# Optimization experiments

Hardware: AMD Instinct MI355X
Metric: run time of the kernel (lower is better)

The kernel has to match this reference:

```python
import jax, jax.numpy as jnp
import numpy as np
from jax import lax


def _make_grid():
    # Faithful replication of the torch buffer construction in __init__.
    r = np.arange(-128, 128) * np.pi / 256.0
    X, Y = np.meshgrid(r, r, indexing='ij')            # torch.meshgrid default 'ij'
    grid = np.tile(np.stack([X, Y], 0), (16, 1, 1))    # [32,256,256] channels x,y,x,y,...
    scales = 2.0 ** np.repeat(np.arange(16) / 2.0, 2)  # [32]: f0,f0,f1,f1,...
    grid = np.sin(grid * scales[:, None, None])
    return jnp.asarray(grid.reshape(32, 256 * 256).T, dtype=jnp.float32)  # [65536,32]

IMG_GRID = _make_grid()


def _conv_lrelu(x, w, b, padding, groups):
    y = lax.conv_general_dilated(x, w, (1, 1), padding,
                                 feature_group_count=groups,
                                 dimension_numbers=('NCHW', 'OIHW', 'NCHW'))
    return jax.nn.leaky_relu(y + b[None, :, None, None])


def _wn_linear(x, v, g, b):
    # nn.utils.weight_norm(Linear): w = g * v / ||v||  (norm over input dim, per output row)
    w = v * (g / jnp.linalg.norm(v, axis=1))[:, None]
    return x @ w.T + b


def _mem_stack(x, vf, gf, bf, vg, gg, bg):
    # memcnn AdditiveCoupling: x1,x2 = chunk(x,2); y1 = x1 + Fm(x2); y2 = x2 + Gm(y1)
    def step(h, p):
        pvf, pgf, pbf, pvg, pgg, pbg = p
        h1, h2 = jnp.split(h, 2, axis=-1)
        y1 = h1 + jax.nn.leaky_relu(_wn_linear(h2, pvf, pgf, pbf))
        y2 = h2 + jax.nn.leaky_relu(_wn_linear(y1, pvg, pgg, pbg))
        return jnp.concatenate([y1, y2], axis=-1), None
    h, _ = lax.scan(step, x, (vf, gf, bf, vg, gg, bg))
    return h


def _forward(feature, cw1, cb1, cw2, cb2, cw3, cb3, cw4, cb4, cw5, cb5,
             w1, b1, m1_vf, m1_gf, m1_bf, m1_vg, m1_gg, m1_bg,
             w2, b2, m2_vf, m2_gf, m2_bf, m2_vg, m2_gg, m2_bg, w3, b3):
    B = feature.shape[0]
    h = _conv_lrelu(feature, cw1, cb1, 'SAME', 4)
    h = _conv_lrelu(h, cw2, cb2, 'SAME', 3)
    h = _conv_lrelu(h, cw3, cb3, 'SAME', 2)
    h = _conv_lrelu(h, cw4, cb4, 'VALID', 3)
    h = _conv_lrelu(h, cw5, cb5, 'VALID', 1)   # [B,128,4,4]
    feat = h.reshape(B, -1)                    # [B,2048]
    N = IMG_GRID.shape[0]                      # 65536 coords, fully vectorized (no python chunk loop)
    grid_b = jnp.broadcast_to(IMG_GRID[None], (B, N, 32))
    x = jnp.concatenate([grid_b, jnp.broadcast_to(feat[:, None, :], (B, N, feat.shape[1]))], -1)
    mid = jax.nn.leaky_relu(x @ w1.T + b1)     # [B,N,1024]
    mid = _mem_stack(mid, m1_vf, m1_gf, m1_bf, m1_vg, m1_gg, m1_bg)
    h2 = jax.nn.leaky_relu(jnp.concatenate([grid_b, mid], -1) @ w2.T + b2)  # [B,N,512]
    h2 = _mem_stack(h2, m2_vf, m2_gf, m2_bf, m2_vg, m2_gg, m2_bg)
    rgb = jax.nn.sigmoid(h2 @ w3.T + b3)       # [B,N,3]
    img = rgb.transpose(0, 2, 1).reshape(B, 3, 256, 256)
    return img * 1.1 - 0.05


def setup_inputs() -> dict:
    key = jax.random.key(0)
    ks = iter(jax.random.split(key, 48))
    def nrm(shape, s=0.02):
        return jax.random.normal(next(ks), shape, jnp.float32) * s
    def gpar(shape):
        return jax.random.uniform(next(ks), shape, jnp.float32, 0.5, 1.0)
    inp = {}
    inp['feature'] = jax.random.normal(next(ks), (1, 1792, 8, 8), jnp.float32)
    inp['cw1'] = nrm((768, 448, 3, 3)); inp['cb1'] = nrm((768,), 0.01)   # groups=4: 1792/4=448
    inp['cw2'] = nrm((768, 256, 3, 3)); inp['cb2'] = nrm((768,), 0.01)   # groups=3
    inp['cw3'] = nrm((768, 384, 3, 3)); inp['cb3'] = nrm((768,), 0.01)   # groups=2
    inp['cw4'] = nrm((768, 256, 3, 3)); inp['cb4'] = nrm((768,), 0.01)   # groups=3, valid
    inp['cw5'] = nrm((128, 768, 3, 3)); inp['cb5'] = nrm((128,), 0.01)   # groups=1, valid
    inp['w1'] = nrm((1024, 2080)); inp['b1'] = nrm((1024,), 0.01)
    inp['m1_vf'] = nrm((8, 512, 512), 1.0); inp['m1_gf'] = gpar((8, 512)); inp['m1_bf'] = nrm((8, 512), 0.01)
    inp['m1_vg'] = nrm((8, 512, 512), 1.0); inp['m1_gg'] = gpar((8, 512)); inp['m1_bg'] = nrm((8, 512), 0.01)
    inp['w2'] = nrm((512, 1056)); inp['b2'] = nrm((512,), 0.01)
    inp['m2_vf'] = nrm((8, 256, 256), 1.0); inp['m2_gf'] = gpar((8, 256)); inp['m2_bf'] = nrm((8, 256), 0.01)
    inp['m2_vg'] = nrm((8, 256, 256), 1.0); inp['m2_gg'] = gpar((8, 256)); inp['m2_bg'] = nrm((8, 256), 0.01)
    inp['w3'] = nrm((3, 512)); inp['b3'] = nrm((3,), 0.01)
    return inp


def reference(feature, cw1, cb1, cw2, cb2, cw3, cb3, cw4, cb4, cw5, cb5,
              w1, b1, m1_vf, m1_gf, m1_bf, m1_vg, m1_gg, m1_bg,
              w2, b2, m2_vf, m2_gf, m2_bf, m2_vg, m2_gg, m2_bg, w3, b3):
    return _forward(feature, cw1, cb1, cw2, cb2, cw3, cb3, cw4, cb4, cw5, cb5,
                    w1, b1, m1_vf, m1_gf, m1_bf, m1_vg, m1_gg, m1_bg,
                    w2, b2, m2_vf, m2_gf, m2_bf, m2_vg, m2_gg, m2_bg, w3, b3)
```

## Files before the change

### kernel.cpp

```cpp
#include <hip/hip_runtime.h>
#include <cmath>

#define LRELU(x) fmaxf((x), 0.01f * (x))

typedef __attribute__((ext_vector_type(8))) short short8;
typedef __attribute__((ext_vector_type(4))) float f32x4;
typedef __attribute__((ext_vector_type(2))) unsigned uint2v;

constexpr int RS = 1032;

__device__ __forceinline__ unsigned short f2bf(float f) {
    return __builtin_bit_cast(unsigned short, (__bf16)f);
}
__device__ __forceinline__ float bf2f(unsigned short h) {
    return __uint_as_float((unsigned)h << 16);
}
__device__ __forceinline__ unsigned pk2(unsigned short a, unsigned short b) {
    return (unsigned)a | ((unsigned)b << 16);
}

__global__ void sgrid_kernel(float* __restrict__ sg) {
    int idx = blockIdx.x * blockDim.x + threadIdx.x;
    if (idx >= 256 * 32) return;
    int t = idx >> 5, c = idx & 31;
    double r = (double)(t - 128) * 3.14159265358979323846 / 256.0;
    double scale = exp2(0.5 * (double)(c >> 1));
    sg[idx] = (float)sin(r * scale);
}

__global__ __launch_bounds__(256) void conv_part(
    const float* __restrict__ x, const float* __restrict__ w,
    float* __restrict__ y, int Cin_g, int Cout_g, int Hin, int pad) {
    __shared__ float wsh[64 * 9];
    __shared__ float red[256];
    int oc = blockIdx.x, ch = blockIdx.y;
    int Hout = pad ? Hin : Hin - 2;
    int t = threadIdx.x;
    int ic0 = ch * 64;
    int nic = min(64, Cin_g - ic0);
    const float* wb = w + ((size_t)oc * Cin_g + ic0) * 9;
    for (int i = t; i < nic * 9; i += 256) wsh[i] = wb[i];
    __syncthreads();
    int p = t & 63, sub = t >> 6;
    int oy = p / Hout, ox = p % Hout;
    int g = oc / Cout_g;
    const float* xb = x + ((size_t)g * Cin_g + ic0) * Hin * Hin;
    bool valid = p < Hout * Hout;
    float acc = 0.f;
    if (valid) {
        for (int ic = sub; ic < nic; ic += 4) {
            const float* xc = xb + (size_t)ic * Hin * Hin;
            const float* wc = wsh + ic * 9;
            #pragma unroll
            for (int ky = 0; ky < 3; ++ky) {
                int iy = oy + ky - pad;
                if (iy < 0 || iy >= Hin) continue;
                #pragma unroll
                for (int kx = 0; kx < 3; ++kx) {
                    int ix = ox + kx - pad;
                    if (ix < 0 || ix >= Hin) continue;
                    acc = fmaf(xc[iy * Hin + ix], wc[ky * 3 + kx], acc);
                }
            }
        }
    }
    red[t] = acc;
    __syncthreads();
    if (t < 64 && valid)
        atomicAdd(&y[(size_t)oc * Hout * Hout + p],
                  red[t] + red[t + 64] + red[t + 128] + red[t + 192]);
}

__global__ void conv_finalize(float* __restrict__ y, const float* __restrict__ bias,
                              int HH, int n) {
    int i = blockIdx.x * 256 + threadIdx.x;
    if (i >= n) return;
    float v = y[i] + bias[i / HH];
    y[i] = LRELU(v);
}

__global__ void feat_c1_kernel(const float* __restrict__ feat, const float* __restrict__ w1,
                               const float* __restrict__ b1, float* __restrict__ c1) {
    int o = (blockIdx.x * blockDim.x + threadIdx.x) >> 6;
    int lane = threadIdx.x & 63;
    if (o >= 1024) return;
    const float* wr = w1 + (size_t)o * 2080 + 32;
    float sum = 0.f;
    for (int k = lane; k < 2048; k += 64) sum += feat[k] * wr[k];
    #pragma unroll
    for (int off = 32; off; off >>= 1) sum += __shfl_xor(sum, off);
    if (lane == 0) c1[o] = sum + b1[o];
}

__global__ __launch_bounds__(256) void wn_scale(const float* __restrict__ v, const float* __restrict__ g,
                                                float* __restrict__ s, int K) {
    __shared__ float red[256];
    int r = blockIdx.x, t = threadIdx.x;
    const float* vr = v + (size_t)r * K;
    float sum = 0.f;
    for (int k = t; k < K; k += 256) { float x = vr[k]; sum = fmaf(x, x, sum); }
    red[t] = sum;
    __syncthreads();
    for (int o = 128; o; o >>= 1) {
        if (t < o) red[t] += red[t + o];
        __syncthreads();
    }
    if (t == 0) s[r] = g[r] / sqrtf(red[0]);
}

__global__ void repack_kernel(const float* __restrict__ v, unsigned short* __restrict__ dst,
                              int T, int N, int K, int NT, int ldk, int koff) {
    int W = N / (NT * 16);
    int KC = K / 32;
    size_t total = (size_t)T * W * NT * KC * 64;
    size_t fi = (size_t)blockIdx.x * 256 + threadIdx.x;
    if (fi >= total) return;
    int l = fi & 63;
    size_t r = fi >> 6;
    int kc = r % KC; r /= KC;
    int nt = r % NT; r /= NT;
    int w  = r % W;  r /= W;
    int t  = (int)r;
    int n = w * NT * 16 + nt * 16 + (l & 15);
    int k = kc * 32 + (l >> 4) * 8;
    const float* src = v + ((size_t)t * N + n) * ldk + koff + k;
    unsigned short* d = dst + fi * 8;
    #pragma unroll
    for (int e = 0; e < 8; ++e) d[e] = f2bf(src[e]);
}

__global__ void repack_w2k(const float* __restrict__ w2, unsigned short* __restrict__ dst) {
    int fi = blockIdx.x * 256 + threadIdx.x;
    if (fi >= 65536) return;
    int l = fi & 63;
    int r = fi >> 6;
    int kc = r & 31; r >>= 5;
    int nt = r & 3;  r >>= 2;
    int w = r;
    int l15 = l & 15;
    int col = (nt < 2) ? (w * 32 + nt * 16 + l15) : (256 + w * 32 + (nt - 2) * 16 + l15);
    int k = kc * 32 + (l >> 4) * 8;
    const float* src = w2 + (size_t)col * 1056 + 32 + k;
    unsigned short* d = dst + (size_t)fi * 8;
    #pragma unroll
    for (int e = 0; e < 8; ++e) d[e] = f2bf(src[e]);
}

__global__ void pxy_kernel(const float* __restrict__ sg, const float* __restrict__ w1,
                           const float* __restrict__ c1, float* __restrict__ Px,
                           float* __restrict__ Py) {
    int idx = blockIdx.x * 256 + threadIdx.x;
    int t = idx >> 10, o = idx & 1023;
    const float* wr = w1 + (size_t)o * 2080;
    const float* sr = sg + t * 32;
    float px = 0.f, py = 0.f;
    #pragma unroll
    for (int k = 0; k < 16; ++k) {
        px = fmaf(sr[2 * k], wr[2 * k], px);
        py = fmaf(sr[2 * k + 1], wr[2 * k + 1], py);
    }
    Px[idx] = px + c1[o];
    Py[idx] = py;
}

__global__ void qxy_kernel(const float* __restrict__ sg, const float* __restrict__ w2,
                           float* __restrict__ Qx, float* __restrict__ Qy) {
    int idx = blockIdx.x * 256 + threadIdx.x;
    int t = idx >> 9, o = idx & 511;
    const float* wr = w2 + (size_t)o * 1056;
    const float* sr = sg + t * 32;
    float qx = 0.f, qy = 0.f;
    #pragma unroll
    for (int k = 0; k < 16; ++k) {
        qx = fmaf(sr[2 * k], wr[2 * k], qx);
        qy = fmaf(sr[2 * k + 1], wr[2 * k + 1], qy);
    }
    Qx[idx] = qx;
    Qy[idx] = qy;
}

__device__ __forceinline__ void step1(unsigned short* sm, int w, int l, int l15, int lq,
                                      int srcb, int dstb,
                                      const unsigned short* __restrict__ Bp,
                                      const float* __restrict__ sc,
                                      const float* __restrict__ bi,
                                      f32x4* master) {
    f32x4 acc[4][4] = {};
    const unsigned short* wb = Bp + (size_t)w * (4 * 16 * 512) + (size_t)l * 8;
    const unsigned short* abase = sm + (size_t)l15 * RS + srcb + lq * 8;
    short8 b0[4], b1[4];
    #pragma unroll
    for (int nt = 0; nt < 4; ++nt) b0[nt] = *(const short8*)(wb + (size_t)(nt * 16 + 0) * 512);
    #pragma unroll
    for (int nt = 0; nt < 4; ++nt) b1[nt] = *(const short8*)(wb + (size_t)(nt * 16 + 1) * 512);
    #pragma unroll
    for (int kc = 0; kc < 16; ++kc) {
        short8 bn[4];
        if (kc < 14) {
            #pragma unroll
            for (int nt = 0; nt < 4; ++nt)
                bn[nt] = *(const short8*)(wb + (size_t)(nt * 16 + kc + 2) * 512);
        }
        short8 af[4];
        #pragma unroll
        for (int mt = 0; mt < 4; ++mt)
            af[mt] = *(const short8*)(abase + (size_t)(mt * 16) * RS + kc * 32);
        #pragma unroll
        for (int mt = 0; mt < 4; ++mt)
            #pragma unroll
            for (int nt = 0; nt < 4; ++nt)
                acc[mt][nt] = __builtin_amdgcn_mfma_f32_16x16x32_bf16(b0[nt], af[mt], acc[mt][nt], 0, 0, 0);
        #pragma unroll
        for (int nt = 0; nt < 4; ++nt) { b0[nt] = b1[nt]; b1[nt] = bn[nt]; }
    }
    #pragma unroll
    for (int nt = 0; nt < 4; ++nt) {
        int nb = w * 64 + nt * 16 + lq * 4;
        float4 s4 = *(const float4*)(sc + nb);
        float4 bb = *(const float4*)(bi + nb);
        #pragma unroll
        for (int mt = 0; mt < 4; ++mt) {
            int row = mt * 16 + l15;
            f32x4 m = master[mt * 4 + nt];
            float v0 = LRELU(acc[mt][nt][0] * s4.x + bb.x) + m[0];
            float v1 = LRELU(acc[mt][nt][1] * s4.y + bb.y) + m[1];
            float v2 = LRELU(acc[mt][nt][2] * s4.z + bb.z) + m[2];
            float v3 = LRELU(acc[mt][nt][3] * s4.w + bb.w) + m[3];
            m[0] = v0; m[1] = v1; m[2] = v2; m[3] = v3;
            master[mt * 4 + nt] = m;
            uint2v hv; hv[0] = pk2(f2bf(v0), f2bf(v1)); hv[1] = pk2(f2bf(v2), f2bf(v3));
            *(uint2v*)(sm + (size_t)row * RS + dstb + nb) = hv;
        }
    }
}

__device__ __forceinline__ void step2(unsigned short* sm, int w, int l, int l15, int lq,
                                      int srcb, int dstb,
                                      const unsigned short* __restrict__ Bp,
                                      const float* __restrict__ sc,
                                      const float* __restrict__ bi,
                                      f32x4* master) {
    f32x4 acc[4][2] = {};
    const unsigned short* wb = Bp + (size_t)w * (2 * 8 * 512) + (size_t)l * 8;
    const unsigned short* abase = sm + (size_t)l15 * RS + srcb + lq * 8;
    short8 b0[2], b1[2];
    #pragma unroll
    for (int nt = 0; nt < 2; ++nt) b0[nt] = *(const short8*)(wb + (size_t)(nt * 8 + 0) * 512);
    #pragma unroll
    for (int nt = 0; nt < 2; ++nt) b1[nt] = *(const short8*)(wb + (size_t)(nt * 8 + 1) * 512);
    #pragma unroll
    for (int kc = 0; kc < 8; ++kc) {
        short8 bn[2];
        if (kc < 6) {
            #pragma unroll
            for (int nt = 0; nt < 2; ++nt)
                bn[nt] = *(const short8*)(wb + (size_t)(nt * 8 + kc + 2) * 512);
        }
        short8 af[4];
        #pragma unroll
        for (int mt = 0; mt < 4; ++mt)
            af[mt] = *(const short8*)(abase + (size_t)(mt * 16) * RS + kc * 32);
        #pragma unroll
        for (int mt = 0; mt < 4; ++mt)
            #pragma unroll
            for (int nt = 0; nt < 2; ++nt)
                acc[mt][nt] = __builtin_amdgcn_mfma_f32_16x16x32_bf16(b0[nt], af[mt], acc[mt][nt], 0, 0, 0);
        #pragma unroll
        for (int nt = 0; nt < 2; ++nt) { b0[nt] = b1[nt]; b1[nt] = bn[nt]; }
    }
    #pragma unroll
    for (int nt = 0; nt < 2; ++nt) {
        int nb = w * 32 + nt * 16 + lq * 4;
        float4 s4 = *(const float4*)(sc + nb);
        float4 bb = *(const float4*)(bi + nb);
        #pragma unroll
        for (int mt = 0; mt < 4; ++mt) {
            int row = mt * 16 + l15;
            f32x4 m = master[mt * 2 + nt];
            float v0 = LRELU(acc[mt][nt][0] * s4.x + bb.x) + m[0];
            float v1 = LRELU(acc[mt][nt][1] * s4.y + bb.y) + m[1];
            float v2 = LRELU(acc[mt][nt][2] * s4.z + bb.z) + m[2];
            float v3 = LRELU(acc[mt][nt][3] * s4.w + bb.w) + m[3];
            m[0] = v0; m[1] = v1; m[2] = v2; m[3] = v3;
            master[mt * 2 + nt] = m;
            uint2v hv; hv[0] = pk2(f2bf(v0), f2bf(v1)); hv[1] = pk2(f2bf(v2), f2bf(v3));
            *(uint2v*)(sm + (size_t)row * RS + dstb + nb) = hv;
        }
    }
}

__global__ __launch_bounds__(512, 2) void fused_mlp(
    const float* __restrict__ Px, const float* __restrict__ Py,
    const float* __restrict__ Qx, const float* __restrict__ Qy,
    const unsigned short* __restrict__ m1f, const float* __restrict__ s1f, const float* __restrict__ bf1,
    const unsigned short* __restrict__ m1g, const float* __restrict__ s1g, const float* __restrict__ bg1,
    const unsigned short* __restrict__ w2m, const float* __restrict__ b2,
    const unsigned short* __restrict__ m2f, const float* __restrict__ s2f, const float* __restrict__ bf2_,
    const unsigned short* __restrict__ m2g, const float* __restrict__ s2g, const float* __restrict__ bg2_,
    const float* __restrict__ w3, const float* __restrict__ b3,
    float* __restrict__ out) {
    extern __shared__ unsigned short sm[];
    int tid = threadIdx.x;
    int w = tid >> 6, l = tid & 63;
    int l15 = l & 15, lq = l >> 4;
    int n0 = blockIdx.x * 64;
    int i = n0 >> 8, jb = n0 & 255;

    f32x4 mh[32];

    #pragma unroll
    for (int h = 0; h < 2; ++h) {
        #pragma unroll
        for (int nt = 0; nt < 4; ++nt) {
            int nb = h * 512 + w * 64 + nt * 16 + lq * 4;
            float4 px4 = *(const float4*)(Px + (size_t)i * 1024 + nb);
            #pragma unroll
            for (int mt = 0; mt < 4; ++mt) {
                int row = mt * 16 + l15;
                float4 py4 = *(const float4*)(Py + (size_t)(jb + row) * 1024 + nb);
                f32x4 m;
                m[0] = LRELU(px4.x + py4.x);
                m[1] = LRELU(px4.y + py4.y);
                m[2] = LRELU(px4.z + py4.z);
                m[3] = LRELU(px4.w + py4.w);
                mh[h * 16 + mt * 4 + nt] = m;
                uint2v hv; hv[0] = pk2(f2bf(m[0]), f2bf(m[1])); hv[1] = pk2(f2bf(m[2]), f2bf(m[3]));
                *(uint2v*)(sm + (size_t)row * RS + nb) = hv;
            }
        }
    }
    __syncthreads();

    for (int t = 0; t < 8; ++t) {
        step1(sm, w, l, l15, lq, 512, 0, m1f + (size_t)t * 512 * 512, s1f + t * 512, bf1 + t * 512, mh);
        __syncthreads();
        step1(sm, w, l, l15, lq, 0, 512, m1g + (size_t)t * 512 * 512, s1g + t * 512, bg1 + t * 512, mh + 16);
        __syncthreads();
    }

    {
        f32x4 acc[4][4] = {};
        const unsigned short* wb = w2m + (size_t)w * (4 * 32 * 512) + (size_t)l * 8;
        const unsigned short* abase = sm + (size_t)l15 * RS + lq * 8;
        short8 b0[4], b1[4];
        #pragma unroll
        for (int nt = 0; nt < 4; ++nt) b0[nt] = *(const short8*)(wb + (size_t)(nt * 32 + 0) * 512);
        #pragma unroll
        for (int nt = 0; nt < 4; ++nt) b1[nt] = *(const short8*)(wb + (size_t)(nt * 32 + 1) * 512);
        #pragma unroll
        for (int kc = 0; kc < 32; ++kc) {
            short8 bn[4];
            if (kc < 30) {
                #pragma unroll
                for (int nt = 0; nt < 4; ++nt)
                    bn[nt] = *(const short8*)(wb + (size_t)(nt * 32 + kc + 2) * 512);
            }
            short8 af[4];
            #pragma unroll
            for (int mt = 0; mt < 4; ++mt)
                af[mt] = *(const short8*)(abase + (size_t)(mt * 16) * RS + kc * 32);
            #pragma unroll
            for (int mt = 0; mt < 4; ++mt)
                #pragma unroll
                for (int nt = 0; nt < 4; ++nt)
                    acc[mt][nt] = __builtin_amdgcn_mfma_f32_16x16x32_bf16(b0[nt], af[mt], acc[mt][nt], 0, 0, 0);
            #pragma unroll
            for (int nt = 0; nt < 4; ++nt) { b0[nt] = b1[nt]; b1[nt] = bn[nt]; }
        }
        __syncthreads();
        #pragma unroll
        for (int nt = 0; nt < 4; ++nt) {
            int colb = ((nt < 2) ? (w * 32 + nt * 16) : (256 + w * 32 + (nt - 2) * 16)) + lq * 4;
            float4 qx4 = *(const float4*)(Qx + (size_t)i * 512 + colb);
            float4 b24 = *(const float4*)(b2 + colb);
            #pragma unroll
            for (int mt = 0; mt < 4; ++mt) {
                int row = mt * 16 + l15;
                float4 qy4 = *(const float4*)(Qy + (size_t)(jb + row) * 512 + colb);
                f32x4 m;
                m[0] = LRELU(acc[mt][nt][0] + qx4.x + qy4.x + b24.x);
                m[1] = LRELU(acc[mt][nt][1] + qx4.y + qy4.y + b24.y);
                m[2] = LRELU(acc[mt][nt][2] + qx4.z + qy4.z + b24.z);
                m[3] = LRELU(acc[mt][nt][3] + qx4.w + qy4.w + b24.w);
                mh[(nt >> 1) * 16 + mt * 2 + (nt & 1)] = m;
                uint2v hv; hv[0] = pk2(f2bf(m[0]), f2bf(m[1])); hv[1] = pk2(f2bf(m[2]), f2bf(m[3]));
                *(uint2v*)(sm + (size_t)row * RS + colb) = hv;
            }
        }
    }
    __syncthreads();

    for (int t = 0; t < 8; ++t) {
        step2(sm, w, l, l15, lq, 256, 0, m2f + (size_t)t * 256 * 256, s2f + t * 256, bf2_ + t * 256, mh);
        __syncthreads();
        step2(sm, w, l, l15, lq, 0, 256, m2g + (size_t)t * 256 * 256, s2g + t * 256, bg2_ + t * 256, mh + 16);
        __syncthreads();
    }

    __syncthreads();
    {
        float* smf = (float*)sm;
        #pragma unroll
        for (int hh = 0; hh < 2; ++hh)
            #pragma unroll
            for (int nt = 0; nt < 2; ++nt) {
                int colb = hh * 256 + w * 32 + nt * 16 + lq * 4;
                #pragma unroll
                for (int mt = 0; mt < 4; ++mt) {
                    int row = mt * 16 + l15;
                    f32x4 m = mh[hh * 16 + mt * 2 + nt];
                    *(f32x4*)(smf + (size_t)row * (RS / 2) + colb) = m;
                }
            }
    }
    __syncthreads();
    {
        const float* smf = (const float*)sm;
        #pragma unroll
        for (int rr = 0; rr < 8; ++rr) {
            int row = w * 8 + rr;
            float s0 = 0.f, s1 = 0.f, s2 = 0.f;
            #pragma unroll
            for (int it = 0; it < 8; ++it) {
                int k = it * 64 + l;
                float hv = smf[(size_t)row * (RS / 2) + k];
                s0 = fmaf(hv, w3[k], s0);
                s1 = fmaf(hv, w3[512 + k], s1);
                s2 = fmaf(hv, w3[1024 + k], s2);
            }
            #pragma unroll
            for (int off = 32; off; off >>= 1) {
                s0 += __shfl_xor(s0, off);
                s1 += __shfl_xor(s1, off);
                s2 += __shfl_xor(s2, off);
            }
            if (l == 0) {
                float v[3] = {s0 + b3[0], s1 + b3[1], s2 + b3[2]};
                #pragma unroll
                for (int c = 0; c < 3; ++c) {
                    float sg = 1.0f / (1.0f + expf(-v[c]));
                    out[(size_t)c * 65536 + n0 + row] = 1.1f * sg - 0.05f;
                }
            }
        }
    }
}

extern "C" void kernel_launch(void* const* d_in, const int* in_sizes, int n_in,
                              void* d_out, int out_size, void* d_ws, size_t ws_size,
                              hipStream_t stream) {
    const float* feature = (const float*)d_in[0];
    const float* cw1 = (const float*)d_in[1];  const float* cb1 = (const float*)d_in[2];
    const float* cw2 = (const float*)d_in[3];  const float* cb2 = (const float*)d_in[4];
    const float* cw3 = (const float*)d_in[5];  const float* cb3 = (const float*)d_in[6];
    const float* cw4 = (const float*)d_in[7];  const float* cb4 = (const float*)d_in[8];
    const float* cw5 = (const float*)d_in[9];  const float* cb5 = (const float*)d_in[10];
    const float* w1  = (const float*)d_in[11]; const float* b1  = (const float*)d_in[12];
    const float* m1_vf = (const float*)d_in[13]; const float* m1_gf = (const float*)d_in[14];
    const float* m1_bf = (const float*)d_in[15];
    const float* m1_vg = (const float*)d_in[16]; const float* m1_gg = (const float*)d_in[17];
    const float* m1_bg = (const float*)d_in[18];
    const float* w2  = (const float*)d_in[19]; const float* b2  = (const float*)d_in[20];
    const float* m2_vf = (const float*)d_in[21]; const float* m2_gf = (const float*)d_in[22];
    const float* m2_bf = (const float*)d_in[23];
    const float* m2_vg = (const float*)d_in[24]; const float* m2_gg = (const float*)d_in[25];
    const float* m2_bg = (const float*)d_in[26];
    const float* w3  = (const float*)d_in[27]; const float* b3  = (const float*)d_in[28];
    float* out = (float*)d_out;

    float* ws = (float*)d_ws;
    size_t off = 0;
    float* sgrid   = ws + off; off += 256 * 32;
    float* cbA     = ws + off; off += 768 * 64;
    float* cbB     = ws + off; off += 768 * 64;
    float* featbuf = ws + off; off += 2048;
    float* c1      = ws + off; off += 1024;
    float* s1f     = ws + off; off += 8 * 512;
    float* s1g     = ws + off; off += 8 * 512;
    float* s2f     = ws + off; off += 8 * 256;
    float* s2g     = ws + off; off += 8 * 256;
    float* Px      = ws + off; off += 256 * 1024;
    float* Py      = ws + off; off += 256 * 1024;
    float* Qx      = ws + off; off += 256 * 512;
    float* Qy      = ws + off; off += 256 * 512;
    unsigned short* m1f_p = (unsigned short*)(ws + off); off += (size_t)8 * 512 * 512 / 2;
    unsigned short* m1g_p = (unsigned short*)(ws + off); off += (size_t)8 * 512 * 512 / 2;
    unsigned short* m2f_p = (unsigned short*)(ws + off); off += (size_t)8 * 256 * 256 / 2;
    unsigned short* m2g_p = (unsigned short*)(ws + off); off += (size_t)8 * 256 * 256 / 2;
    unsigned short* w2m_p = (unsigned short*)(ws + off); off += (size_t)512 * 1024 / 2;

    sgrid_kernel<<<32, 256, 0, stream>>>(sgrid);
    wn_scale<<<8 * 512, 256, 0, stream>>>(m1_vf, m1_gf, s1f, 512);
    wn_scale<<<8 * 512, 256, 0, stream>>>(m1_vg, m1_gg, s1g, 512);
    wn_scale<<<8 * 256, 256, 0, stream>>>(m2_vf, m2_gf, s2f, 256);
    wn_scale<<<8 * 256, 256, 0, stream>>>(m2_vg, m2_gg, s2g, 256);
    repack_kernel<<<1024, 256, 0, stream>>>(m1_vf, m1f_p, 8, 512, 512, 4, 512, 0);
    repack_kernel<<<1024, 256, 0, stream>>>(m1_vg, m1g_p, 8, 512, 512, 4, 512, 0);
    repack_kernel<<<256, 256, 0, stream>>>(m2_vf, m2f_p, 8, 256, 256, 2, 256, 0);
    repack_kernel<<<256, 256, 0, stream>>>(m2_vg, m2g_p, 8, 256, 256, 2, 256, 0);
    repack_w2k<<<256, 256, 0, stream>>>(w2, w2m_p);

    hipMemsetAsync(cbA, 0, 768 * 64 * sizeof(float), stream);
    conv_part<<<dim3(768, 7), 256, 0, stream>>>(feature, cw1, cbA, 448, 192, 8, 1);
    conv_finalize<<<(768 * 64) / 256, 256, 0, stream>>>(cbA, cb1, 64, 768 * 64);
    hipMemsetAsync(cbB, 0, 768 * 64 * sizeof(float), stream);
    conv_part<<<dim3(768, 4), 256, 0, stream>>>(cbA, cw2, cbB, 256, 256, 8, 1);
    conv_finalize<<<(768 * 64) / 256, 256, 0, stream>>>(cbB, cb2, 64, 768 * 64);
    hipMemsetAsync(cbA, 0, 768 * 64 * sizeof(float), stream);
    conv_part<<<dim3(768, 6), 256, 0, stream>>>(cbB, cw3, cbA, 384, 384, 8, 1);
    conv_finalize<<<(768 * 64) / 256, 256, 0, stream>>>(cbA, cb3, 64, 768 * 64);
    hipMemsetAsync(cbB, 0, 768 * 36 * sizeof(float), stream);
    conv_part<<<dim3(768, 4), 256, 0, stream>>>(cbA, cw4, cbB, 256, 256, 8, 0);
    conv_finalize<<<(768 * 36 + 255) / 256, 256, 0, stream>>>(cbB, cb4, 36, 768 * 36);
    hipMemsetAsync(featbuf, 0, 2048 * sizeof(float), stream);
    conv_part<<<dim3(128, 12), 256, 0, stream>>>(cbB, cw5, featbuf, 768, 128, 6, 0);
    conv_finalize<<<(2048 + 255) / 256, 256, 0, stream>>>(featbuf, cb5, 16, 2048);

    feat_c1_kernel<<<1024 / 4, 256, 0, stream>>>(featbuf, w1, b1, c1);
    pxy_kernel<<<(256 * 1024) / 256, 256, 0, stream>>>(sgrid, w1, c1, Px, Py);
    qxy_kernel<<<(256 * 512) / 256, 256, 0, stream>>>(sgrid, w2, Qx, Qy);

    size_t lds_bytes = (size_t)64 * RS * sizeof(unsigned short);
    hipFuncSetAttribute(reinterpret_cast<const void*>(fused_mlp),
                        hipFuncAttributeMaxDynamicSharedMemorySize, (int)lds_bytes);
    fused_mlp<<<1024, 512, lds_bytes, stream>>>(
        Px, Py, Qx, Qy,
        m1f_p, s1f, m1_bf, m1g_p, s1g, m1_bg,
        w2m_p, b2,
        m2f_p, s2f, m2_bf, m2g_p, s2g, m2_bg,
        w3, b3, out);
}
```

Measured before the change: 1.428 ms.

## Store fp32 residual stream as bf16 hi/lo pairs; merge setup kernels and memsets

The residual master copy of the coupling-block state in the fused MLP kernel changes from fp32 registers (32 f32x4) to a split bf16 hi+lo representation. For the first stack, the hi half sits in LDS and the lo half in packed registers. For the second stack, both halves sit in LDS, so the final projection reads them straight from shared memory with no fp32 staging pass. Setup kernels (weight-norm scales, repacks, P/Q precompute) are merged into single launches and the conv memsets collapse into one, cutting launch count. The aim is lower register pressure and fewer launches, at the cost of extra LDS traffic and pack/unpack ALU work per step, plus a small precision change from the two-bf16 approximation of fp32.

```diff
diff --git a/kernel.cpp b/kernel.cpp
--- a/kernel.cpp
+++ b/kernel.cpp
@@ -12,11 +12,25 @@
 __device__ __forceinline__ unsigned short f2bf(float f) {
     return __builtin_bit_cast(unsigned short, (__bf16)f);
 }
-__device__ __forceinline__ float bf2f(unsigned short h) {
-    return __uint_as_float((unsigned)h << 16);
-}
 __device__ __forceinline__ unsigned pk2(unsigned short a, unsigned short b) {
     return (unsigned)a | ((unsigned)b << 16);
+}
+__device__ __forceinline__ uint2v cvt4(f32x4 v) {
+    uint2v r;
+    r[0] = pk2(f2bf(v[0]), f2bf(v[1]));
+    r[1] = pk2(f2bf(v[2]), f2bf(v[3]));
+    return r;
+}
+__device__ __forceinline__ f32x4 unpk4(uint2v p) {
+    f32x4 r;
+    r[0] = __uint_as_float(p[0] << 16);
+    r[1] = __uint_as_float(p[0] & 0xffff0000u);
+    r[2] = __uint_as_float(p[1] << 16);
+    r[3] = __uint_as_float(p[1] & 0xffff0000u);
+    return r;
+}
+__device__ __forceinline__ f32x4 lrelu4(f32x4 v) {
+    return __builtin_elementwise_max(v, 0.01f * v);
 }
 
 __global__ void sgrid_kernel(float* __restrict__ sg) {
@@ -92,10 +106,18 @@
     if (lane == 0) c1[o] = sum + b1[o];
 }
 
-__global__ __launch_bounds__(256) void wn_scale(const float* __restrict__ v, const float* __restrict__ g,
-                                                float* __restrict__ s, int K) {
+__global__ __launch_bounds__(256) void wn_all(
+    const float* __restrict__ v1f, const float* __restrict__ g1f, float* __restrict__ s1f,
+    const float* __restrict__ v1g, const float* __restrict__ g1g, float* __restrict__ s1g,
+    const float* __restrict__ v2f, const float* __restrict__ g2f, float* __restrict__ s2f,
+    const float* __restrict__ v2g, const float* __restrict__ g2g, float* __restrict__ s2g) {
     __shared__ float red[256];
-    int r = blockIdx.x, t = threadIdx.x;
+    int b = blockIdx.x, t = threadIdx.x;
+    const float* v; const float* g; float* s; int K, r;
+    if (b < 4096)       { v = v1f; g = g1f; s = s1f; K = 512; r = b; }
+    else if (b < 8192)  { v = v1g; g = g1g; s = s1g; K = 512; r = b - 4096; }
+    else if (b < 10240) { v = v2f; g = g2f; s = s2f; K = 256; r = b - 8192; }
+    else                { v = v2g; g = g2g; s = s2g; K = 256; r = b - 10240; }
     const float* vr = v + (size_t)r * K;
     float sum = 0.f;
     for (int k = t; k < K; k += 256) { float x = vr[k]; sum = fmaf(x, x, sum); }
@@ -108,14 +130,10 @@
     if (t == 0) s[r] = g[r] / sqrtf(red[0]);
 }
 
-__global__ void repack_kernel(const float* __restrict__ v, unsigned short* __restrict__ dst,
-                              int T, int N, int K, int NT, int ldk, int koff) {
+__device__ __forceinline__ void repack_one(const float* __restrict__ v, unsigned short* __restrict__ dst,
+                                           int N, int NT, int KC, int ldk, int koff, size_t fi) {
     int W = N / (NT * 16);
-    int KC = K / 32;
-    size_t total = (size_t)T * W * NT * KC * 64;
-    size_t fi = (size_t)blockIdx.x * 256 + threadIdx.x;
-    if (fi >= total) return;
-    int l = fi & 63;
+    int l = (int)(fi & 63);
     size_t r = fi >> 6;
     int kc = r % KC; r /= KC;
     int nt = r % NT; r /= NT;
@@ -129,54 +147,52 @@
     for (int e = 0; e < 8; ++e) d[e] = f2bf(src[e]);
 }
 
-__global__ void repack_w2k(const float* __restrict__ w2, unsigned short* __restrict__ dst) {
-    int fi = blockIdx.x * 256 + threadIdx.x;
-    if (fi >= 65536) return;
-    int l = fi & 63;
-    int r = fi >> 6;
-    int kc = r & 31; r >>= 5;
-    int nt = r & 3;  r >>= 2;
-    int w = r;
-    int l15 = l & 15;
-    int col = (nt < 2) ? (w * 32 + nt * 16 + l15) : (256 + w * 32 + (nt - 2) * 16 + l15);
-    int k = kc * 32 + (l >> 4) * 8;
-    const float* src = w2 + (size_t)col * 1056 + 32 + k;
-    unsigned short* d = dst + (size_t)fi * 8;
-    #pragma unroll
-    for (int e = 0; e < 8; ++e) d[e] = f2bf(src[e]);
-}
-
-__global__ void pxy_kernel(const float* __restrict__ sg, const float* __restrict__ w1,
-                           const float* __restrict__ c1, float* __restrict__ Px,
-                           float* __restrict__ Py) {
+__global__ void repack_all(const float* __restrict__ m1vf, const float* __restrict__ m1vg,
+                           const float* __restrict__ m2vf, const float* __restrict__ m2vg,
+                           const float* __restrict__ w2,
+                           unsigned short* __restrict__ p1f, unsigned short* __restrict__ p1g,
+                           unsigned short* __restrict__ p2f, unsigned short* __restrict__ p2g,
+                           unsigned short* __restrict__ pw2) {
+    size_t fi = (size_t)blockIdx.x * 256 + threadIdx.x;
+    const size_t n1 = 262144, n2 = 65536;
+    if (fi < n1)                repack_one(m1vf, p1f, 512, 4, 16, 512, 0, fi);
+    else if (fi < 2 * n1)       repack_one(m1vg, p1g, 512, 4, 16, 512, 0, fi - n1);
+    else if (fi < 2 * n1 + n2)  repack_one(m2vf, p2f, 256, 2, 8, 256, 0, fi - 2 * n1);
+    else if (fi < 2 * n1 + 2 * n2) repack_one(m2vg, p2g, 256, 2, 8, 256, 0, fi - 2 * n1 - n2);
+    else                        repack_one(w2, pw2, 512, 4, 32, 1056, 32, fi - 2 * n1 - 2 * n2);
+}
+
+__global__ void pq_kernel(const float* __restrict__ sg, const float* __restrict__ w1,
+                          const float* __restrict__ c1, const float* __restrict__ w2,
+                          float* __restrict__ Px, float* __restrict__ Py,
+                          float* __restrict__ Qx, float* __restrict__ Qy) {
     int idx = blockIdx.x * 256 + threadIdx.x;
-    int t = idx >> 10, o = idx & 1023;
-    const float* wr = w1 + (size_t)o * 2080;
-    const float* sr = sg + t * 32;
-    float px = 0.f, py = 0.f;
-    #pragma unroll
-    for (int k = 0; k < 16; ++k) {
-        px = fmaf(sr[2 * k], wr[2 * k], px);
-        py = fmaf(sr[2 * k + 1], wr[2 * k + 1], py);
-    }
-    Px[idx] = px + c1[o];
-    Py[idx] = py;
-}
-
-__global__ void qxy_kernel(const float* __restrict__ sg, const float* __restrict__ w2,
-                           float* __restrict__ Qx, float* __restrict__ Qy) {
-    int idx = blockIdx.x * 256 + threadIdx.x;
-    int t = idx >> 9, o = idx & 511;
-    const float* wr = w2 + (size_t)o * 1056;
-    const float* sr = sg + t * 32;
-    float qx = 0.f, qy = 0.f;
-    #pragma unroll
-    for (int k = 0; k < 16; ++k) {
-        qx = fmaf(sr[2 * k], wr[2 * k], qx);
-        qy = fmaf(sr[2 * k + 1], wr[2 * k + 1], qy);
-    }
-    Qx[idx] = qx;
-    Qy[idx] = qy;
+    if (idx < 256 * 1024) {
+        int t = idx >> 10, o = idx & 1023;
+        const float* wr = w1 + (size_t)o * 2080;
+        const float* sr = sg + t * 32;
+        float px = 0.f, py = 0.f;
+        #pragma unroll
+        for (int k = 0; k < 16; ++k) {
+            px = fmaf(sr[2 * k], wr[2 * k], px);
+            py = fmaf(sr[2 * k + 1], wr[2 * k + 1], py);
+        }
+        Px[idx] = px + c1[o];
+        Py[idx] = py;
+    } else {
+        int j = idx - 256 * 1024;
+        int t = j >> 9, o = j & 511;
+        const float* wr = w2 + (size_t)o * 1056;
+        const float* sr = sg + t * 32;
+        float qx = 0.f, qy = 0.f;
+        #pragma unroll
+        for (int k = 0; k < 16; ++k) {
+            qx = fmaf(sr[2 * k], wr[2 * k], qx);
+            qy = fmaf(sr[2 * k + 1], wr[2 * k + 1], qy);
+        }
+        Qx[j] = qx;
+        Qy[j] = qy;
+    }
 }
 
 __device__ __forceinline__ void step1(unsigned short* sm, int w, int l, int l15, int lq,
@@ -184,7 +200,7 @@
                                       const unsigned short* __restrict__ Bp,
                                       const float* __restrict__ sc,
                                       const float* __restrict__ bi,
-                                      f32x4* master) {
+                                      uint2v* lo_half) {
     f32x4 acc[4][4] = {};
     const unsigned short* wb = Bp + (size_t)w * (4 * 16 * 512) + (size_t)l * 8;
     const unsigned short* abase = sm + (size_t)l15 * RS + srcb + lq * 8;
@@ -216,20 +232,18 @@
     #pragma unroll
     for (int nt = 0; nt < 4; ++nt) {
         int nb = w * 64 + nt * 16 + lq * 4;
-        float4 s4 = *(const float4*)(sc + nb);
-        float4 bb = *(const float4*)(bi + nb);
+        f32x4 s4 = *(const f32x4*)(sc + nb);
+        f32x4 bb = *(const f32x4*)(bi + nb);
         #pragma unroll
         for (int mt = 0; mt < 4; ++mt) {
             int row = mt * 16 + l15;
-            f32x4 m = master[mt * 4 + nt];
-            float v0 = LRELU(acc[mt][nt][0] * s4.x + bb.x) + m[0];
-            float v1 = LRELU(acc[mt][nt][1] * s4.y + bb.y) + m[1];
-            float v2 = LRELU(acc[mt][nt][2] * s4.z + bb.z) + m[2];
-            float v3 = LRELU(acc[mt][nt][3] * s4.w + bb.w) + m[3];
-            m[0] = v0; m[1] = v1; m[2] = v2; m[3] = v3;
-            master[mt * 4 + nt] = m;
-            uint2v hv; hv[0] = pk2(f2bf(v0), f2bf(v1)); hv[1] = pk2(f2bf(v2), f2bf(v3));
-            *(uint2v*)(sm + (size_t)row * RS + dstb + nb) = hv;
+            size_t hidx = (size_t)row * RS + dstb + nb;
+            uint2v hold = *(uint2v*)(sm + hidx);
+            f32x4 v = lrelu4(acc[mt][nt] * s4 + bb);
+            v += unpk4(hold) + unpk4(lo_half[mt * 4 + nt]);
+            uint2v hnew = cvt4(v);
+            *(uint2v*)(sm + hidx) = hnew;
+            lo_half[mt * 4 + nt] = cvt4(v - unpk4(hnew));
         }
     }
 }
@@ -238,8 +252,7 @@
                                       int srcb, int dstb,
                                       const unsigned short* __restrict__ Bp,
                                       const float* __restrict__ sc,
-                                      const float* __restrict__ bi,
-                                      f32x4* master) {
+                                      const float* __restrict__ bi) {
     f32x4 acc[4][2] = {};
     const unsigned short* wb = Bp + (size_t)w * (2 * 8 * 512) + (size_t)l * 8;
     const unsigned short* abase = sm + (size_t)l15 * RS + srcb + lq * 8;
@@ -271,20 +284,19 @@
     #pragma unroll
     for (int nt = 0; nt < 2; ++nt) {
         int nb = w * 32 + nt * 16 + lq * 4;
-        float4 s4 = *(const float4*)(sc + nb);
-        float4 bb = *(const float4*)(bi + nb);
+        f32x4 s4 = *(const f32x4*)(sc + nb);
+        f32x4 bb = *(const f32x4*)(bi + nb);
         #pragma unroll
         for (int mt = 0; mt < 4; ++mt) {
             int row = mt * 16 + l15;
-            f32x4 m = master[mt * 2 + nt];
-            float v0 = LRELU(acc[mt][nt][0] * s4.x + bb.x) + m[0];
-            float v1 = LRELU(acc[mt][nt][1] * s4.y + bb.y) + m[1];
-            float v2 = LRELU(acc[mt][nt][2] * s4.z + bb.z) + m[2];
-            float v3 = LRELU(acc[mt][nt][3] * s4.w + bb.w) + m[3];
-            m[0] = v0; m[1] = v1; m[2] = v2; m[3] = v3;
-            master[mt * 2 + nt] = m;
-            uint2v hv; hv[0] = pk2(f2bf(v0), f2bf(v1)); hv[1] = pk2(f2bf(v2), f2bf(v3));
-            *(uint2v*)(sm + (size_t)row * RS + dstb + nb) = hv;
+            size_t hidx = (size_t)row * RS + dstb + nb;
+            uint2v hold = *(uint2v*)(sm + hidx);
+            uint2v lold = *(uint2v*)(sm + hidx + 512);
+            f32x4 v = lrelu4(acc[mt][nt] * s4 + bb);
+            v += unpk4(hold) + unpk4(lold);
+            uint2v hnew = cvt4(v);
+            *(uint2v*)(sm + hidx) = hnew;
+            *(uint2v*)(sm + hidx + 512) = cvt4(v - unpk4(hnew));
         }
     }
 }
@@ -306,35 +318,31 @@
     int n0 = blockIdx.x * 64;
     int i = n0 >> 8, jb = n0 & 255;
 
-    f32x4 mh[32];
+    uint2v lo_pk[32];
 
     #pragma unroll
     for (int h = 0; h < 2; ++h) {
         #pragma unroll
         for (int nt = 0; nt < 4; ++nt) {
             int nb = h * 512 + w * 64 + nt * 16 + lq * 4;
-            float4 px4 = *(const float4*)(Px + (size_t)i * 1024 + nb);
+            f32x4 px4 = *(const f32x4*)(Px + (size_t)i * 1024 + nb);
             #pragma unroll
             for (int mt = 0; mt < 4; ++mt) {
                 int row = mt * 16 + l15;
-                float4 py4 = *(const float4*)(Py + (size_t)(jb + row) * 1024 + nb);
-                f32x4 m;
-                m[0] = LRELU(px4.x + py4.x);
-                m[1] = LRELU(px4.y + py4.y);
-                m[2] = LRELU(px4.z + py4.z);
-                m[3] = LRELU(px4.w + py4.w);
-                mh[h * 16 + mt * 4 + nt] = m;
-                uint2v hv; hv[0] = pk2(f2bf(m[0]), f2bf(m[1])); hv[1] = pk2(f2bf(m[2]), f2bf(m[3]));
+                f32x4 py4 = *(const f32x4*)(Py + (size_t)(jb + row) * 1024 + nb);
+                f32x4 v = lrelu4(px4 + py4);
+                uint2v hv = cvt4(v);
                 *(uint2v*)(sm + (size_t)row * RS + nb) = hv;
+                lo_pk[h * 16 + mt * 4 + nt] = cvt4(v - unpk4(hv));
             }
         }
     }
     __syncthreads();
 
     for (int t = 0; t < 8; ++t) {
-        step1(sm, w, l, l15, lq, 512, 0, m1f + (size_t)t * 512 * 512, s1f + t * 512, bf1 + t * 512, mh);
+        step1(sm, w, l, l15, lq, 512, 0, m1f + (size_t)t * 512 * 512, s1f + t * 512, bf1 + t * 512, lo_pk);
         __syncthreads();
-        step1(sm, w, l, l15, lq, 0, 512, m1g + (size_t)t * 512 * 512, s1g + t * 512, bg1 + t * 512, mh + 16);
+        step1(sm, w, l, l15, lq, 0, 512, m1g + (size_t)t * 512 * 512, s1g + t * 512, bg1 + t * 512, lo_pk + 16);
         __syncthreads();
     }
 
@@ -370,77 +378,56 @@
         __syncthreads();
         #pragma unroll
         for (int nt = 0; nt < 4; ++nt) {
-            int colb = ((nt < 2) ? (w * 32 + nt * 16) : (256 + w * 32 + (nt - 2) * 16)) + lq * 4;
-            float4 qx4 = *(const float4*)(Qx + (size_t)i * 512 + colb);
-            float4 b24 = *(const float4*)(b2 + colb);
+            int nb = w * 64 + nt * 16 + lq * 4;
+            f32x4 qx4 = *(const f32x4*)(Qx + (size_t)i * 512 + nb);
+            f32x4 b24 = *(const f32x4*)(b2 + nb);
             #pragma unroll
             for (int mt = 0; mt < 4; ++mt) {
                 int row = mt * 16 + l15;
-                float4 qy4 = *(const float4*)(Qy + (size_t)(jb + row) * 512 + colb);
-                f32x4 m;
-                m[0] = LRELU(acc[mt][nt][0] + qx4.x + qy4.x + b24.x);
-                m[1] = LRELU(acc[mt][nt][1] + qx4.y + qy4.y + b24.y);
-                m[2] = LRELU(acc[mt][nt][2] + qx4.z + qy4.z + b24.z);
-                m[3] = LRELU(acc[mt][nt][3] + qx4.w + qy4.w + b24.w);
-                mh[(nt >> 1) * 16 + mt * 2 + (nt & 1)] = m;
-                uint2v hv; hv[0] = pk2(f2bf(m[0]), f2bf(m[1])); hv[1] = pk2(f2bf(m[2]), f2bf(m[3]));
-                *(uint2v*)(sm + (size_t)row * RS + colb) = hv;
+                f32x4 qy4 = *(const f32x4*)(Qy + (size_t)(jb + row) * 512 + nb);
+                f32x4 v = lrelu4(acc[mt][nt] + qx4 + qy4 + b24);
+                uint2v hv = cvt4(v);
+                size_t hidx = (size_t)row * RS + nb;
+                *(uint2v*)(sm + hidx) = hv;
+                *(uint2v*)(sm + hidx + 512) = cvt4(v - unpk4(hv));
             }
         }
     }
     __syncthreads();
 
     for (int t = 0; t < 8; ++t) {
-        step2(sm, w, l, l15, lq, 256, 0, m2f + (size_t)t * 256 * 256, s2f + t * 256, bf2_ + t * 256, mh);
+        step2(sm, w, l, l15, lq, 256, 0, m2f + (size_t)t * 256 * 256, s2f + t * 256, bf2_ + t * 256);
         __syncthreads();
-        step2(sm, w, l, l15, lq, 0, 256, m2g + (size_t)t * 256 * 256, s2g + t * 256, bg2_ + t * 256, mh + 16);
+        step2(sm, w, l, l15, lq, 0, 256, m2g + (size_t)t * 256 * 256, s2g + t * 256, bg2_ + t * 256);
         __syncthreads();
     }
 
-    __syncthreads();
-    {
-        float* smf = (float*)sm;
-        #pragma unroll
-        for (int hh = 0; hh < 2; ++hh)
-            #pragma unroll
-            for (int nt = 0; nt < 2; ++nt) {
-                int colb = hh * 256 + w * 32 + nt * 16 + lq * 4;
-                #pragma unroll
-                for (int mt = 0; mt < 4; ++mt) {
-                    int row = mt * 16 + l15;
-                    f32x4 m = mh[hh * 16 + mt * 2 + nt];
-                    *(f32x4*)(smf + (size_t)row * (RS / 2) + colb) = m;
-                }
-            }
-    }
-    __syncthreads();
-    {
-        const float* smf = (const float*)sm;
-        #pragma unroll
-        for (int rr = 0; rr < 8; ++rr) {
-            int row = w * 8 + rr;
-            float s0 = 0.f, s1 = 0.f, s2 = 0.f;
-            #pragma unroll
-            for (int it = 0; it < 8; ++it) {
-                int k = it * 64 + l;
-                float hv = smf[(size_t)row * (RS / 2) + k];
-                s0 = fmaf(hv, w3[k], s0);
-                s1 = fmaf(hv, w3[512 + k], s1);
-                s2 = fmaf(hv, w3[1024 + k], s2);
-            }
-            #pragma unroll
-            for (int off = 32; off; off >>= 1) {
-                s0 += __shfl_xor(s0, off);
-                s1 += __shfl_xor(s1, off);
-                s2 += __shfl_xor(s2, off);
-            }
-            if (l == 0) {
-                float v[3] = {s0 + b3[0], s1 + b3[1], s2 + b3[2]};
-                #pragma unroll
-                for (int c = 0; c < 3; ++c) {
-                    float sg = 1.0f / (1.0f + expf(-v[c]));
-                    out[(size_t)c * 65536 + n0 + row] = 1.1f * sg - 0.05f;
-                }
+    #pragma unroll
+    for (int rr = 0; rr < 8; ++rr) {
+        int row = w * 8 + rr;
+        float s0 = 0.f, s1 = 0.f, s2 = 0.f;
+        #pragma unroll
+        for (int it = 0; it < 8; ++it) {
+            int k = it * 64 + l;
+            size_t hidx = (size_t)row * RS + k;
+            float hv = __uint_as_float((unsigned)sm[hidx] << 16) +
+                       __uint_as_float((unsigned)sm[hidx + 512] << 16);
+            s0 = fmaf(hv, w3[k], s0);
+            s1 = fmaf(hv, w3[512 + k], s1);
+            s2 = fmaf(hv, w3[1024 + k], s2);
+        }
+        #pragma unroll
+        for (int off = 32; off; off >>= 1) {
+            s0 += __shfl_xor(s0, off);
+            s1 += __shfl_xor(s1, off);
+            s2 += __shfl_xor(s2, off);
+        }
+        if (l == 0) {
+            float v[3] = {s0 + b3[0], s1 + b3[1], s2 + b3[2]};
+            #pragma unroll
+            for (int c = 0; c < 3; ++c) {
+                float sg = 1.0f / (1.0f + expf(-v[c]));
+                out[(size_t)c * 65536 + n0 + row] = 1.1f * sg - 0.05f;
             }
         }
     }
@@ -473,7 +460,10 @@
     float* sgrid   = ws + off; off += 256 * 32;
     float* cbA     = ws + off; off += 768 * 64;
     float* cbB     = ws + off; off += 768 * 64;
+    float* cbC     = ws + off; off += 768 * 64;
+    float* cbD     = ws + off; off += 768 * 36;
     float* featbuf = ws + off; off += 2048;
+    size_t convN   = 768 * 64 * 3 + 768 * 36 + 2048;
     float* c1      = ws + off; off += 1024;
     float* s1f     = ws + off; off += 8 * 512;
     float* s1g     = ws + off; off += 8 * 512;
@@ -490,35 +480,25 @@
     unsigned short* w2m_p = (unsigned short*)(ws + off); off += (size_t)512 * 1024 / 2;
 
     sgrid_kernel<<<32, 256, 0, stream>>>(sgrid);
-    wn_scale<<<8 * 512, 256, 0, stream>>>(m1_vf, m1_gf, s1f, 512);
-    wn_scale<<<8 * 512, 256, 0, stream>>>(m1_vg, m1_gg, s1g, 512);
-    wn_scale<<<8 * 256, 256, 0, stream>>>(m2_vf, m2_gf, s2f, 256);
-    wn_scale<<<8 * 256, 256, 0, stream>>>(m2_vg, m2_gg, s2g, 256);
-    repack_kernel<<<1024, 256, 0, stream>>>(m1_vf, m1f_p, 8, 512, 512, 4, 512, 0);
-    repack_kernel<<<1024, 256, 0, stream>>>(m1_vg, m1g_p, 8, 512, 512, 4, 512, 0);
-    repack_kernel<<<256, 256, 0, stream>>>(m2_vf, m2f_p, 8, 256, 256, 2, 256, 0);
-    repack_kernel<<<256, 256, 0, stream>>>(m2_vg, m2g_p, 8, 256, 256, 2, 256, 0);
-    repack_w2k<<<256, 256, 0, stream>>>(w2, w2m_p);
-
-    hipMemsetAsync(cbA, 0, 768 * 64 * sizeof(float), stream);
+    wn_all<<<12288, 256, 0, stream>>>(m1_vf, m1_gf, s1f, m1_vg, m1_gg, s1g,
+                                      m2_vf, m2_gf, s2f, m2_vg, m2_gg, s2g);
+    repack_all<<<2816, 256, 0, stream>>>(m1_vf, m1_vg, m2_vf, m2_vg, w2,
+                                         m1f_p, m1g_p, m2f_p, m2g_p, w2m_p);
+
+    hipMemsetAsync(cbA, 0, convN * sizeof(float), stream);
     conv_part<<<dim3(768, 7), 256, 0, stream>>>(feature, cw1, cbA, 448, 192, 8, 1);
     conv_finalize<<<(768 * 64) / 256, 256, 0, stream>>>(cbA, cb1, 64, 768 * 64);
-    hipMemsetAsync(cbB, 0, 768 * 64 * sizeof(float), stream);
     conv_part<<<dim3(768, 4), 256, 0, stream>>>(cbA, cw2, cbB, 256, 256, 8, 1);
     conv_finalize<<<(768 * 64) / 256, 256, 0, stream>>>(cbB, cb2, 64, 768 * 64);
-    hipMemsetAsync(cbA, 0, 768 * 64 * sizeof(float), stream);
-    conv_part<<<dim3(768, 6), 256, 0, stream>>>(cbB, cw3, cbA, 384, 384, 8, 1);
-    conv_finalize<<<(768 * 64) / 256, 256, 0, stream>>>(cbA, cb3, 64, 768 * 64);
-    hipMemsetAsync(cbB, 0, 768 * 36 * sizeof(float), stream);
-    conv_part<<<dim3(768, 4), 256, 0, stream>>>(cbA, cw4, cbB, 256, 256, 8, 0);
-    conv_finalize<<<(768 * 36 + 255) / 256, 256, 0, stream>>>(cbB, cb4, 36, 768 * 36);
-    hipMemsetAsync(featbuf, 0, 2048 * sizeof(float), stream);
-    conv_part<<<dim3(128, 12), 256, 0, stream>>>(cbB, cw5, featbuf, 768, 128, 6, 0);
+    conv_part<<<dim3(768, 6), 256, 0, stream>>>(cbB, cw3, cbC, 384, 384, 8, 1);
+    conv_finalize<<<(768 * 64) / 256, 256, 0, stream>>>(cbC, cb3, 64, 768 * 64);
+    conv_part<<<dim3(768, 4), 256, 0, stream>>>(cbC, cw4, cbD, 256, 256, 8, 0);
+    conv_finalize<<<(768 * 36 + 255) / 256, 256, 0, stream>>>(cbD, cb4, 36, 768 * 36);
+    conv_part<<<dim3(128, 12), 256, 0, stream>>>(cbD, cw5, featbuf, 768, 128, 6, 0);
     conv_finalize<<<(2048 + 255) / 256, 256, 0, stream>>>(featbuf, cb5, 16, 2048);
 
     feat_c1_kernel<<<1024 / 4, 256, 0, stream>>>(featbuf, w1, b1, c1);
-    pxy_kernel<<<(256 * 1024) / 256, 256, 0, stream>>>(sgrid, w1, c1, Px, Py);
-    qxy_kernel<<<(256 * 512) / 256, 256, 0, stream>>>(sgrid, w2, Qx, Qy);
+    pq_kernel<<<(256 * 1024 + 256 * 512) / 256, 256, 0, stream>>>(sgrid, w1, c1, w2, Px, Py, Qx, Qy);
 
     size_t lds_bytes = (size_t)64 * RS * sizeof(unsigned short);
     hipFuncSetAttribute(reinterpret_cast<const void*>(fused_mlp),
```

Result: faster. 1.282 ms (-10.2%).
